# Performance work log

Hardware: AMD Instinct MI355X
Metric: run time of the kernel (lower is better)

The kernel has to match this reference:

```python
import jax, jax.numpy as jnp
import numpy as np

T = 8          # time steps (init kwarg T)
GAMA = 1.0     # ZIF surrogate width (init kwarg gama)
LR = 0.1       # adaptive-threshold learning rate (init kwarg learning_rate)
THRESH = 8.0   # init kwarg thresh

# ZIF spiking activation: heaviside forward, triangular surrogate backward
@jax.custom_vjp
def heaviside(u):
    return (u >= 0).astype(u.dtype)

def _hv_fwd(u):
    return (u >= 0).astype(u.dtype), u

def _hv_bwd(u, g):
    surr = (1.0 / GAMA) * (1.0 / GAMA) * jnp.maximum(GAMA - jnp.abs(u), 0.0)
    return (g * surr,)

heaviside.defvjp(_hv_fwd, _hv_bwd)


def setup_inputs() -> dict:
    key = jax.random.key(0)
    x = jax.random.normal(key, (T * 32, 128, 32, 32), dtype=jnp.float32)  # [T*B, C, H, W]
    thresh = jnp.full((1,), THRESH, dtype=jnp.float32)                    # learnable thresh param
    return {"x": x, "thresh": thresh}


def reference(x, thresh):
    # thresh is used via .data in torch -> detached
    thre = jax.lax.stop_gradient(thresh)[0]
    B = x.shape[0] // T
    xs = x.reshape((T, B) + x.shape[1:])           # [T, B, C, H, W]
    C = xs.shape[2]
    neuron_thre0 = jnp.full((C,), thre, x.dtype)   # per-channel threshold init
    cur = neuron_thre0.reshape(1, C, 1, 1)         # broadcasts over [B, C, H, W]

    # sequential IF recurrence over T, carrying membrane potential
    def step(mem, xt):
        mem = mem + xt
        s = heaviside(mem - cur)
        mem = mem - s * cur
        return mem, s

    mem0 = jnp.broadcast_to(0.5 * cur, xs.shape[1:]).astype(x.dtype)
    mem, spikes = jax.lax.scan(step, mem0, xs)     # spikes: [T, B, C, H, W]

    # compensation pass over the stacked spike history
    compen_mem = mem - 0.5 * cur
    spike_count = spikes.sum(axis=0)               # [B, C, H, W]
    compen_value = jnp.minimum(compen_mem + spike_count * cur, T * cur)
    pos = (compen_value > 0) & (spike_count > 0)
    safe_count = jnp.where(spike_count > 0, spike_count, jnp.ones_like(spike_count))
    new_thre = jnp.where(pos, compen_value / safe_count, jnp.zeros_like(compen_value))

    # adaptive threshold update (scalar gradient-descent style step)
    ub = new_thre.mean(axis=(0, 2, 3))             # [C] per-channel target
    diff = ub - neuron_thre0
    mask = jax.lax.stop_gradient((neuron_thre0 > ub).astype(x.dtype))
    update = LR * 2.0 * (diff * mask).mean()       # scalar
    neuron_thre = neuron_thre0 + update            # [C]

    # scale spikes by the updated per-channel threshold, merge temporal dim
    out = spikes * neuron_thre.reshape(1, 1, C, 1, 1)
    return out.reshape((T * B,) + x.shape[1:])
```

## Files before the change

kernel.cpp:

```cpp
#include <hip/hip_runtime.h>
#include <stdint.h>

static constexpr int   T_    = 8;
static constexpr int   C_    = 128;
static constexpr int   N_    = 32 * 128 * 32 * 32;
static constexpr int   N4_   = N_ / 4;
static constexpr int   NBLK_ = N_ / 4 / 256;
static constexpr float LR_   = 0.1f;

typedef float v4f __attribute__((ext_vector_type(4)));

template <bool PACK>
__global__ __launch_bounds__(256) void k_fwd(const float* __restrict__ x,
                                             const float* __restrict__ thresh,
                                             uint8_t* __restrict__ spk,
                                             float* __restrict__ part) {
    const float thre = thresh[0];
    const int e4   = blockIdx.x * 256 + threadIdx.x;
    const int base = e4 * 4;
    float    mem[4];
    unsigned pb[4] = {0, 0, 0, 0};
#pragma unroll
    for (int i = 0; i < 4; ++i) mem[i] = 0.5f * thre;
#pragma unroll
    for (int t = 0; t < T_; ++t) {
        const v4f xv = *reinterpret_cast<const v4f*>(x + (size_t)t * N_ + base);
#pragma unroll
        for (int i = 0; i < 4; ++i) {
            mem[i] += xv[i];
            if (mem[i] - thre >= 0.0f) {
                mem[i] -= thre;
                pb[i] |= (1u << t);
            }
        }
    }
    if (PACK) {
        __builtin_nontemporal_store(
            pb[0] | (pb[1] << 8) | (pb[2] << 16) | (pb[3] << 24),
            reinterpret_cast<unsigned*>(spk) + e4);
    }
    float local = 0.0f;
#pragma unroll
    for (int i = 0; i < 4; ++i) {
        const int   cnt = __popc(pb[i]);
        const float compen_mem = mem[i] - 0.5f * thre;
        const float cv = fminf(compen_mem + (float)cnt * thre, (float)T_ * thre);
        if (cv > 0.0f && cnt > 0) local += cv / (float)cnt;
    }
#pragma unroll
    for (int off = 32; off > 0; off >>= 1) local += __shfl_down(local, off, 64);
    __shared__ float wpart[4];
    const int lane = threadIdx.x & 63;
    const int wid  = threadIdx.x >> 6;
    if (lane == 0) wpart[wid] = local;
    __syncthreads();
    if (threadIdx.x == 0) part[blockIdx.x] = wpart[0] + wpart[1] + wpart[2] + wpart[3];
}

__global__ __launch_bounds__(128) void k_scalar(const float* __restrict__ part,
                                                const float* __restrict__ thresh,
                                                float* __restrict__ scal) {
    const float thre = thresh[0];
    float sum = 0.0f;
#pragma unroll
    for (int g = 0; g < NBLK_ / C_; ++g) sum += part[g * C_ + threadIdx.x];
    const float ub = sum * (1.0f / 32768.0f);
    float v = (thre > ub) ? (ub - thre) : 0.0f;
#pragma unroll
    for (int off = 32; off > 0; off >>= 1) v += __shfl_down(v, off, 64);
    __shared__ float partial[2];
    if ((threadIdx.x & 63) == 0) partial[threadIdx.x >> 6] = v;
    __syncthreads();
    if (threadIdx.x == 0) {
        scal[0] = thre + LR_ * 2.0f * (partial[0] + partial[1]) * (1.0f / (float)C_);
    }
}

__global__ __launch_bounds__(256) void k_out_fill(const uint8_t* __restrict__ spk,
                                                  const float* __restrict__ scal,
                                                  float* __restrict__ out) {
    const float s = scal[0];
    const int t = blockIdx.x >> 8;
    const int site4_base = (blockIdx.x & 255) * 4096;
    const unsigned* sp32 = reinterpret_cast<const unsigned*>(spk);
#pragma unroll
    for (int it = 0; it < 16; ++it) {
        const int i4 = it * 256 + threadIdx.x;
        const unsigned p = sp32[site4_base + i4];
        v4f o;
        o.x = ((p >> t) & 1)        ? s : 0.0f;
        o.y = ((p >> (8 + t)) & 1)  ? s : 0.0f;
        o.z = ((p >> (16 + t)) & 1) ? s : 0.0f;
        o.w = ((p >> (24 + t)) & 1) ? s : 0.0f;
        __builtin_nontemporal_store(
            o, reinterpret_cast<v4f*>(out) + (size_t)t * N4_ + site4_base + i4);
    }
}

__global__ __launch_bounds__(256) void k_out_recompute(const float* __restrict__ x,
                                                       const float* __restrict__ thresh,
                                                       const float* __restrict__ scal,
                                                       float* __restrict__ out) {
    const float thre = thresh[0];
    const float s    = scal[0];
    const int e4   = blockIdx.x * 256 + threadIdx.x;
    const int base = e4 * 4;
    float mem[4];
#pragma unroll
    for (int i = 0; i < 4; ++i) mem[i] = 0.5f * thre;
#pragma unroll
    for (int t = 0; t < T_; ++t) {
        const v4f xv = *reinterpret_cast<const v4f*>(x + (size_t)t * N_ + base);
        v4f o;
#pragma unroll
        for (int i = 0; i < 4; ++i) {
            mem[i] += xv[i];
            if (mem[i] - thre >= 0.0f) { mem[i] -= thre; o[i] = s; }
            else                        { o[i] = 0.0f; }
        }
        __builtin_nontemporal_store(o, reinterpret_cast<v4f*>(out + (size_t)t * N_ + base));
    }
}

extern "C" void kernel_launch(void* const* d_in, const int* in_sizes, int n_in,
                              void* d_out, int out_size, void* d_ws, size_t ws_size,
                              hipStream_t stream) {
    const float* x      = (const float*)d_in[0];
    const float* thresh = (const float*)d_in[1];
    float*       out    = (float*)d_out;

    float*   part = (float*)d_ws;
    float*   scal = (float*)((uint8_t*)d_ws + 16384);
    uint8_t* spk  = (uint8_t*)d_ws + 32768;
    const bool pack = ws_size >= (size_t)(32768 + N_);

    if (pack) {
        k_fwd<true><<<NBLK_, 256, 0, stream>>>(x, thresh, spk, part);
        k_scalar<<<1, 128, 0, stream>>>(part, thresh, scal);
        k_out_fill<<<T_ * 256, 256, 0, stream>>>(spk, scal, out);
    } else {
        k_fwd<false><<<NBLK_, 256, 0, stream>>>(x, thresh, nullptr, part);
        k_scalar<<<1, 128, 0, stream>>>(part, thresh, scal);
        k_out_recompute<<<NBLK_, 256, 0, stream>>>(x, thresh, scal, out);
    }
}
```

Before: 54.89 us.

## Fold scalar threshold kernel into output kernel and process 8 elements per thread

Removes the separate single-block scalar kernel. Each output block now recomputes the per-channel mean and the threshold update from the partial sums, which saves one launch and one serialization point. The forward kernel now handles 8 elements per thread and writes two partials per block, one per 1024-element plane, so the per-channel layout stays the same. The cost is redundant small reductions in every output block plus extra syncthreads.

```diff
diff --git a/kernel.cpp b/kernel.cpp
--- a/kernel.cpp
+++ b/kernel.cpp
@@ -5,7 +5,9 @@
 static constexpr int   C_    = 128;
 static constexpr int   N_    = 32 * 128 * 32 * 32;
 static constexpr int   N4_   = N_ / 4;
-static constexpr int   NBLK_ = N_ / 4 / 256;
+static constexpr int   NPLANE_ = N_ / 1024;
+static constexpr int   NBLK1_  = N_ / 8 / 256;
+static constexpr int   NBLKF_  = N_ / 4 / 256;
 static constexpr float LR_   = 0.1f;
 
 typedef float v4f __attribute__((ext_vector_type(4)));
@@ -16,70 +18,89 @@
                                              uint8_t* __restrict__ spk,
                                              float* __restrict__ part) {
     const float thre = thresh[0];
-    const int e4   = blockIdx.x * 256 + threadIdx.x;
-    const int base = e4 * 4;
-    float    mem[4];
-    unsigned pb[4] = {0, 0, 0, 0};
+    const int tid  = threadIdx.x;
+    const int base = (blockIdx.x * 256 + tid) * 8;
+
+    float    mem[8];
+    unsigned pb[8] = {0, 0, 0, 0, 0, 0, 0, 0};
 #pragma unroll
-    for (int i = 0; i < 4; ++i) mem[i] = 0.5f * thre;
+    for (int i = 0; i < 8; ++i) mem[i] = 0.5f * thre;
+
 #pragma unroll
     for (int t = 0; t < T_; ++t) {
-        const v4f xv = *reinterpret_cast<const v4f*>(x + (size_t)t * N_ + base);
+        const v4f xa = *reinterpret_cast<const v4f*>(x + (size_t)t * N_ + base);
+        const v4f xb = *reinterpret_cast<const v4f*>(x + (size_t)t * N_ + base + 4);
 #pragma unroll
         for (int i = 0; i < 4; ++i) {
-            mem[i] += xv[i];
-            if (mem[i] - thre >= 0.0f) {
-                mem[i] -= thre;
-                pb[i] |= (1u << t);
-            }
+            mem[i] += xa[i];
+            if (mem[i] - thre >= 0.0f) { mem[i] -= thre; pb[i] |= (1u << t); }
+        }
+#pragma unroll
+        for (int i = 0; i < 4; ++i) {
+            mem[4 + i] += xb[i];
+            if (mem[4 + i] - thre >= 0.0f) { mem[4 + i] -= thre; pb[4 + i] |= (1u << t); }
         }
     }
+
     if (PACK) {
-        __builtin_nontemporal_store(
-            pb[0] | (pb[1] << 8) | (pb[2] << 16) | (pb[3] << 24),
-            reinterpret_cast<unsigned*>(spk) + e4);
+        typedef unsigned v2u __attribute__((ext_vector_type(2)));
+        v2u pk;
+        pk.x = pb[0] | (pb[1] << 8) | (pb[2] << 16) | (pb[3] << 24);
+        pk.y = pb[4] | (pb[5] << 8) | (pb[6] << 16) | (pb[7] << 24);
+        __builtin_nontemporal_store(pk, reinterpret_cast<v2u*>(spk) + blockIdx.x * 256 + tid);
     }
+
     float local = 0.0f;
 #pragma unroll
-    for (int i = 0; i < 4; ++i) {
+    for (int i = 0; i < 8; ++i) {
         const int   cnt = __popc(pb[i]);
         const float compen_mem = mem[i] - 0.5f * thre;
         const float cv = fminf(compen_mem + (float)cnt * thre, (float)T_ * thre);
         if (cv > 0.0f && cnt > 0) local += cv / (float)cnt;
     }
+
 #pragma unroll
     for (int off = 32; off > 0; off >>= 1) local += __shfl_down(local, off, 64);
     __shared__ float wpart[4];
-    const int lane = threadIdx.x & 63;
-    const int wid  = threadIdx.x >> 6;
+    const int lane = tid & 63;
+    const int wid  = tid >> 6;
     if (lane == 0) wpart[wid] = local;
     __syncthreads();
-    if (threadIdx.x == 0) part[blockIdx.x] = wpart[0] + wpart[1] + wpart[2] + wpart[3];
-}
-
-__global__ __launch_bounds__(128) void k_scalar(const float* __restrict__ part,
-                                                const float* __restrict__ thresh,
-                                                float* __restrict__ scal) {
-    const float thre = thresh[0];
-    float sum = 0.0f;
-#pragma unroll
-    for (int g = 0; g < NBLK_ / C_; ++g) sum += part[g * C_ + threadIdx.x];
-    const float ub = sum * (1.0f / 32768.0f);
-    float v = (thre > ub) ? (ub - thre) : 0.0f;
-#pragma unroll
-    for (int off = 32; off > 0; off >>= 1) v += __shfl_down(v, off, 64);
-    __shared__ float partial[2];
-    if ((threadIdx.x & 63) == 0) partial[threadIdx.x >> 6] = v;
-    __syncthreads();
-    if (threadIdx.x == 0) {
-        scal[0] = thre + LR_ * 2.0f * (partial[0] + partial[1]) * (1.0f / (float)C_);
+    if (tid == 0) {
+        part[2 * blockIdx.x]     = wpart[0] + wpart[1];
+        part[2 * blockIdx.x + 1] = wpart[2] + wpart[3];
     }
 }
 
+__device__ __forceinline__ float compute_scalar(const float* __restrict__ part,
+                                                const float thre, float* s_red) {
+    float v = 0.0f;
+    if (threadIdx.x < C_) {
+        float sum = 0.0f;
+#pragma unroll
+        for (int g = 0; g < NPLANE_ / C_; ++g) sum += part[g * C_ + threadIdx.x];
+        const float ub = sum * (1.0f / 32768.0f);
+        v = (thre > ub) ? (ub - thre) : 0.0f;
+    }
+#pragma unroll
+    for (int off = 32; off > 0; off >>= 1) v += __shfl_down(v, off, 64);
+    if ((threadIdx.x & 63) == 0) s_red[1 + (threadIdx.x >> 6)] = v;
+    __syncthreads();
+    if (threadIdx.x == 0) {
+        s_red[0] = thre + LR_ * 2.0f *
+                   (s_red[1] + s_red[2] + s_red[3] + s_red[4]) * (1.0f / (float)C_);
+    }
+    __syncthreads();
+    return s_red[0];
+}
+
 __global__ __launch_bounds__(256) void k_out_fill(const uint8_t* __restrict__ spk,
-                                                  const float* __restrict__ scal,
+                                                  const float* __restrict__ part,
+                                                  const float* __restrict__ thresh,
                                                   float* __restrict__ out) {
-    const float s = scal[0];
+    __shared__ float s_red[5];
+    const float s = compute_scalar(part, thresh[0], s_red);
+
     const int t = blockIdx.x >> 8;
     const int site4_base = (blockIdx.x & 255) * 4096;
     const unsigned* sp32 = reinterpret_cast<const unsigned*>(spk);
@@ -98,27 +119,33 @@
 }
 
 __global__ __launch_bounds__(256) void k_out_recompute(const float* __restrict__ x,
+                                                       const float* __restrict__ part,
                                                        const float* __restrict__ thresh,
-                                                       const float* __restrict__ scal,
                                                        float* __restrict__ out) {
+    __shared__ float s_red[5];
     const float thre = thresh[0];
-    const float s    = scal[0];
-    const int e4   = blockIdx.x * 256 + threadIdx.x;
-    const int base = e4 * 4;
-    float mem[4];
+    const float s = compute_scalar(part, thre, s_red);
+    const int base = (blockIdx.x * 256 + threadIdx.x) * 8;
+    float mem[8];
 #pragma unroll
-    for (int i = 0; i < 4; ++i) mem[i] = 0.5f * thre;
+    for (int i = 0; i < 8; ++i) mem[i] = 0.5f * thre;
 #pragma unroll
     for (int t = 0; t < T_; ++t) {
-        const v4f xv = *reinterpret_cast<const v4f*>(x + (size_t)t * N_ + base);
-        v4f o;
+        const v4f xa = *reinterpret_cast<const v4f*>(x + (size_t)t * N_ + base);
+        const v4f xb = *reinterpret_cast<const v4f*>(x + (size_t)t * N_ + base + 4);
+        v4f oa, ob;
 #pragma unroll
         for (int i = 0; i < 4; ++i) {
-            mem[i] += xv[i];
-            if (mem[i] - thre >= 0.0f) { mem[i] -= thre; o[i] = s; }
-            else                        { o[i] = 0.0f; }
+            mem[i] += xa[i];
+            if (mem[i] - thre >= 0.0f) { mem[i] -= thre; oa[i] = s; } else oa[i] = 0.0f;
         }
-        __builtin_nontemporal_store(o, reinterpret_cast<v4f*>(out + (size_t)t * N_ + base));
+#pragma unroll
+        for (int i = 0; i < 4; ++i) {
+            mem[4 + i] += xb[i];
+            if (mem[4 + i] - thre >= 0.0f) { mem[4 + i] -= thre; ob[i] = s; } else ob[i] = 0.0f;
+        }
+        __builtin_nontemporal_store(oa, reinterpret_cast<v4f*>(out + (size_t)t * N_ + base));
+        __builtin_nontemporal_store(ob, reinterpret_cast<v4f*>(out + (size_t)t * N_ + base + 4));
     }
 }
 
@@ -130,17 +157,14 @@
     float*       out    = (float*)d_out;
 
     float*   part = (float*)d_ws;
-    float*   scal = (float*)((uint8_t*)d_ws + 16384);
     uint8_t* spk  = (uint8_t*)d_ws + 32768;
     const bool pack = ws_size >= (size_t)(32768 + N_);
 
     if (pack) {
-        k_fwd<true><<<NBLK_, 256, 0, stream>>>(x, thresh, spk, part);
-        k_scalar<<<1, 128, 0, stream>>>(part, thresh, scal);
-        k_out_fill<<<T_ * 256, 256, 0, stream>>>(spk, scal, out);
+        k_fwd<true><<<NBLK1_, 256, 0, stream>>>(x, thresh, spk, part);
+        k_out_fill<<<T_ * 256, 256, 0, stream>>>(spk, part, thresh, out);
     } else {
-        k_fwd<false><<<NBLK_, 256, 0, stream>>>(x, thresh, nullptr, part);
-        k_scalar<<<1, 128, 0, stream>>>(part, thresh, scal);
-        k_out_recompute<<<NBLK_, 256, 0, stream>>>(x, thresh, scal, out);
+        k_fwd<false><<<NBLK1_, 256, 0, stream>>>(x, thresh, nullptr, part);
+        k_out_recompute<<<NBLK1_, 256, 0, stream>>>(x, part, thresh, out);
     }
 }
```

New measurement: 53.01 us. -3.4%, faster.
